# Kernel optimization log

Measured on AMD Instinct MI355X. Metric: run time of the kernel, lower is better.

Reference implementation:

```python
import jax, jax.numpy as jnp
import numpy as np

EMB = 1024
HEADS = 16
HD = EMB // HEADS
EPS = 1e-5

def _ln(x, g, b):
    m = jnp.mean(x, axis=-1, keepdims=True)
    v = jnp.mean((x - m) ** 2, axis=-1, keepdims=True)
    return (x - m) * jax.lax.rsqrt(v + EPS) * g + b

def setup_inputs() -> dict:
    key = jax.random.key(0)
    ks = jax.random.split(key, 12)
    s_in = 1.0 / np.sqrt(EMB)
    s_ff = 1.0 / np.sqrt(4 * EMB)
    return {
        "x": jax.random.normal(ks[0], (2, 2048, EMB), jnp.float32),
        "wq": jax.random.uniform(ks[1], (HEADS, EMB, HD), jnp.float32, -s_in, s_in),
        "wk": jax.random.uniform(ks[2], (HEADS, EMB, HD), jnp.float32, -s_in, s_in),
        "wv": jax.random.uniform(ks[3], (HEADS, EMB, HD), jnp.float32, -s_in, s_in),
        "wo": jax.random.uniform(ks[4], (EMB, EMB), jnp.float32, -s_in, s_in),
        "bo": jax.random.uniform(ks[5], (EMB,), jnp.float32, -s_in, s_in),
        "g1": jnp.ones((EMB,), jnp.float32),
        "b1": jnp.zeros((EMB,), jnp.float32),
        "g2": jnp.ones((EMB,), jnp.float32),
        "b2": jnp.zeros((EMB,), jnp.float32),
        "w1": jax.random.uniform(ks[6], (EMB, 4 * EMB), jnp.float32, -s_in, s_in),
        "bf1": jax.random.uniform(ks[7], (4 * EMB,), jnp.float32, -s_in, s_in),
        "w2": jax.random.uniform(ks[8], (4 * EMB, EMB), jnp.float32, -s_ff, s_ff),
        "bf2": jax.random.uniform(ks[9], (EMB,), jnp.float32, -s_ff, s_ff),
    }

def reference(x, wq, wk, wv, wo, bo, g1, b1, g2, b2, w1, bf1, w2, bf2):
    B, T, C = x.shape
    h = _ln(x, g1, b1)
    # all heads batched: [B,H,T,HD]
    q = jnp.einsum('btc,hcd->bhtd', h, wq)
    k = jnp.einsum('btc,hcd->bhtd', h, wk)
    v = jnp.einsum('btc,hcd->bhtd', h, wv)
    # NOTE: original scales by full emb_size C**-0.5, not head_size
    scores = jnp.einsum('bhtd,bhsd->bhts', q, k) * (C ** -0.5)
    causal = jnp.tril(jnp.ones((T, T), bool))
    scores = jnp.where(causal, scores, -jnp.inf)
    w = jax.nn.softmax(scores, axis=-1)
    attn = jnp.einsum('bhts,bhsd->bhtd', w, v)
    attn = attn.transpose(0, 2, 1, 3).reshape(B, T, C)  # concat heads
    x = x + attn @ wo + bo
    h2 = _ln(x, g2, b2)
    ffn = jax.nn.relu(h2 @ w1 + bf1) @ w2 + bf2
    return x + ffn
```

## Files before the change

### kernel.cpp

```cpp
#include <hip/hip_runtime.h>
#include <hip/hip_bf16.h>

typedef __bf16 bf16x8 __attribute__((ext_vector_type(8)));
typedef float f32x4 __attribute__((ext_vector_type(4)));
typedef short s16x8 __attribute__((ext_vector_type(8)));

#define DEV __device__ __forceinline__

DEV float b2f(unsigned short u) {
  unsigned int x = ((unsigned int)u) << 16;
  return __builtin_bit_cast(float, x);
}
DEV unsigned short f2b(float f) {
  unsigned int x = __builtin_bit_cast(unsigned int, f);
  x += 0x7fffu + ((x >> 16) & 1u);
  return (unsigned short)(x >> 16);
}
DEV unsigned int f2b2(float a, float b) {
  float2 t; t.x = a; t.y = b;
  __hip_bfloat162 v = __float22bfloat162_rn(t);
  unsigned int r;
  __builtin_memcpy(&r, &v, 4);
  return r;
}
DEV f32x4 mfma16(bf16x8 a, bf16x8 b, f32x4 c) {
  return __builtin_amdgcn_mfma_f32_16x16x32_bf16(a, b, c, 0, 0, 0);
}
DEV void gl2lds16(const unsigned short* g, unsigned short* l) {
  __builtin_amdgcn_global_load_lds(
      (const __attribute__((address_space(1))) void*)g,
      (__attribute__((address_space(3))) void*)l, 16, 0, 0);
}

__global__ __launch_bounds__(256)
void transpose_k(const float* __restrict__ in, unsigned short* __restrict__ out,
                 int K, int N, long zin, long zout) {
  __shared__ float tile[32][33];
  in  += (size_t)blockIdx.z * zin;
  out += (size_t)blockIdx.z * zout;
  int n0 = blockIdx.x * 32, k0 = blockIdx.y * 32;
  int tx = threadIdx.x, ty = threadIdx.y;
  #pragma unroll
  for (int i = ty; i < 32; i += 8)
    tile[i][tx] = in[(size_t)(k0 + i) * N + n0 + tx];
  __syncthreads();
  #pragma unroll
  for (int i = ty; i < 32; i += 8)
    out[(size_t)(n0 + i) * K + k0 + tx] = f2b(tile[tx][i]);
}

__global__ __launch_bounds__(256)
void transpose_qkv(const float* __restrict__ wq, const float* __restrict__ wk,
                   const float* __restrict__ wv, unsigned short* __restrict__ out) {
  __shared__ float tile[32][33];
  const int z = blockIdx.z;
  const float* in = (z < 16) ? (wq + (size_t)z * 65536)
                  : (z < 32) ? (wk + (size_t)(z - 16) * 65536)
                             : (wv + (size_t)(z - 32) * 65536);
  unsigned short* o = out + (size_t)z * 65536;
  int n0 = blockIdx.x * 32, k0 = blockIdx.y * 32;
  int tx = threadIdx.x, ty = threadIdx.y;
  #pragma unroll
  for (int i = ty; i < 32; i += 8)
    tile[i][tx] = in[(size_t)(k0 + i) * 64 + n0 + tx];
  __syncthreads();
  #pragma unroll
  for (int i = ty; i < 32; i += 8)
    o[(size_t)(n0 + i) * 1024 + k0 + tx] = f2b(tile[tx][i]);
}

__global__ __launch_bounds__(256)
void ln_kernel(const float* __restrict__ x, const float* __restrict__ g,
               const float* __restrict__ b, unsigned short* __restrict__ o) {
  __shared__ float rs[4];
  __shared__ float rq[4];
  int row = blockIdx.x, tid = threadIdx.x;
  const float* xr = x + (size_t)row * 1024;
  float4 raw = ((const float4*)xr)[tid];
  float s = raw.x + raw.y + raw.z + raw.w;
  float q = raw.x*raw.x + raw.y*raw.y + raw.z*raw.z + raw.w*raw.w;
  #pragma unroll
  for (int off = 32; off > 0; off >>= 1) {
    s += __shfl_down(s, off);
    q += __shfl_down(q, off);
  }
  int wave = tid >> 6;
  if ((tid & 63) == 0) { rs[wave] = s; rq[wave] = q; }
  __syncthreads();
  float ts = rs[0] + rs[1] + rs[2] + rs[3];
  float tq = rq[0] + rq[1] + rq[2] + rq[3];
  float mean = ts * (1.0f/1024.0f);
  float var = tq * (1.0f/1024.0f) - mean*mean;
  float rstd = rsqrtf(var + 1e-5f);
  float4 gr = ((const float4*)g)[tid];
  float4 br = ((const float4*)b)[tid];
  float o0 = (raw.x-mean)*rstd*gr.x + br.x;
  float o1 = (raw.y-mean)*rstd*gr.y + br.y;
  float o2 = (raw.z-mean)*rstd*gr.z + br.z;
  float o3 = (raw.w-mean)*rstd*gr.w + br.w;
  uint2 ov;
  ov.x = f2b2(o0, o1);
  ov.y = f2b2(o2, o3);
  ((uint2*)(o + (size_t)row * 1024))[tid] = ov;
}

template<bool RELU, bool BIAS, bool RESID, bool OUTF32, bool VFUSE>
__global__ __launch_bounds__(256)
void gemm_bt(const unsigned short* __restrict__ A, const unsigned short* __restrict__ Bt,
             const float* __restrict__ bias, const float* __restrict__ resid,
             void* __restrict__ Cv, unsigned short* __restrict__ vT, int M, int N, int K) {
  __shared__ unsigned short As[2][128*32];
  __shared__ unsigned short Bs[2][128*32];
  const int tid = threadIdx.x;
  const int lane = tid & 63;
  const int quad = lane >> 4, l16 = lane & 15;
  const int wave = tid >> 6;
  const int m0 = blockIdx.y * 128, n0 = blockIdx.x * 128;
  const int wm = (wave >> 1) * 64, wn = (wave & 1) * 64;

  f32x4 acc[4][4];
  #pragma unroll
  for (int i = 0; i < 4; ++i)
    #pragma unroll
    for (int j = 0; j < 4; ++j) acc[i][j] = (f32x4){0.f, 0.f, 0.f, 0.f};

  const int srow = tid >> 2;
  const int scol = (tid & 3) * 8;
  const unsigned short* Ab = A + (size_t)m0 * K;
  const unsigned short* Bb = Bt + (size_t)n0 * K;

  auto stage = [&](int buf, int k0) {
    gl2lds16(Ab + (size_t)srow * K + k0 + scol,        &As[buf][tid * 8]);
    gl2lds16(Ab + (size_t)(srow + 64) * K + k0 + scol, &As[buf][2048 + tid * 8]);
    gl2lds16(Bb + (size_t)srow * K + k0 + scol,        &Bs[buf][tid * 8]);
    gl2lds16(Bb + (size_t)(srow + 64) * K + k0 + scol, &Bs[buf][2048 + tid * 8]);
  };

  const int niter = K >> 5;
  stage(0, 0);
  __syncthreads();

  for (int it = 0; it < niter; ++it) {
    const int buf = it & 1;
    if (it + 1 < niter) stage(buf ^ 1, (it + 1) * 32);
    bf16x8 af[4], bfr[4];
    #pragma unroll
    for (int i = 0; i < 4; ++i)
      af[i] = __builtin_bit_cast(bf16x8, *(const s16x8*)&As[buf][(wm + i*16 + l16)*32 + quad*8]);
    #pragma unroll
    for (int j = 0; j < 4; ++j)
      bfr[j] = __builtin_bit_cast(bf16x8, *(const s16x8*)&Bs[buf][(wn + j*16 + l16)*32 + quad*8]);
    #pragma unroll
    for (int i = 0; i < 4; ++i)
      #pragma unroll
      for (int j = 0; j < 4; ++j)
        acc[i][j] = mfma16(af[i], bfr[j], acc[i][j]);
    __syncthreads();
  }

  if (VFUSE && n0 >= 2048) {
    #pragma unroll
    for (int i = 0; i < 4; ++i) {
      const int row = m0 + wm + i*16 + quad*4;
      const int b = row >> 11, tloc = row & 2047;
      #pragma unroll
      for (int j = 0; j < 4; ++j) {
        const int col = n0 + wn + j*16 + l16;
        const int h = (col - 2048) >> 6, d = col & 63;
        ushort4 pk;
        pk.x = f2b(acc[i][j][0]);
        pk.y = f2b(acc[i][j][1]);
        pk.z = f2b(acc[i][j][2]);
        pk.w = f2b(acc[i][j][3]);
        *(ushort4*)&vT[((size_t)((b*16 + h)*64 + d))*2048 + tloc] = pk;
      }
    }
    return;
  }

  #pragma unroll
  for (int i = 0; i < 4; ++i) {
    const int row = m0 + wm + i*16 + quad*4;
    #pragma unroll
    for (int j = 0; j < 4; ++j) {
      const int col = n0 + wn + j*16 + l16;
      float bv = 0.f;
      if (BIAS) bv = bias[col];
      #pragma unroll
      for (int r = 0; r < 4; ++r) {
        float v = acc[i][j][r] + bv;
        if (RESID) v += resid[(size_t)(row + r) * N + col];
        if (RELU) v = fmaxf(v, 0.f);
        if (OUTF32) ((float*)Cv)[(size_t)(row + r) * N + col] = v;
        else ((unsigned short*)Cv)[(size_t)(row + r) * N + col] = f2b(v);
      }
    }
  }
}

__global__ __launch_bounds__(256)
void gemm_n1024(const unsigned short* __restrict__ A, const unsigned short* __restrict__ Bt,
                const float* __restrict__ bias, const float* __restrict__ resid,
                float* __restrict__ C, int M, int N, int K) {
  __shared__ unsigned short As[3][64*64];
  __shared__ unsigned short Bs[3][128*64];
  const int tid = threadIdx.x;
  const int lane = tid & 63;
  const int quad = lane >> 4, l16 = lane & 15;
  const int wave = tid >> 6;
  const int id = blockIdx.x;
  const int xcd = id & 7, i2 = id >> 3;
  const int mt = (xcd << 3) | (i2 >> 3);
  const int nt = i2 & 7;
  const int m0 = mt * 64, n0 = nt * 128;
  const int wm = (wave >> 1) * 32, wn = (wave & 1) * 64;

  f32x4 acc[2][4];
  #pragma unroll
  for (int i = 0; i < 2; ++i)
    #pragma unroll
    for (int j = 0; j < 4; ++j) acc[i][j] = (f32x4){0.f, 0.f, 0.f, 0.f};

  const int srow = tid >> 3;
  const int scc  = ((tid & 7) ^ (srow & 7)) * 8;
  const unsigned short* Ab = A + (size_t)m0 * K;
  const unsigned short* Bb = Bt + (size_t)n0 * K;

  auto stage = [&](int buf, int k0) {
    unsigned short* Ad = &As[buf][0];
    unsigned short* Bd = &Bs[buf][0];
    gl2lds16(Ab + (size_t)srow * K + k0 + scc,         Ad + tid * 8);
    gl2lds16(Ab + (size_t)(srow + 32) * K + k0 + scc,  Ad + 2048 + tid * 8);
    gl2lds16(Bb + (size_t)srow * K + k0 + scc,         Bd + tid * 8);
    gl2lds16(Bb + (size_t)(srow + 32) * K + k0 + scc,  Bd + 2048 + tid * 8);
    gl2lds16(Bb + (size_t)(srow + 64) * K + k0 + scc,  Bd + 4096 + tid * 8);
    gl2lds16(Bb + (size_t)(srow + 96) * K + k0 + scc,  Bd + 6144 + tid * 8);
  };

  const int niter = K >> 6;
  stage(0, 0);
  stage(1, 64);

  int bufc = 0;
  for (int it = 0; it < niter; ++it) {
    if (it + 1 < niter) {
      asm volatile("s_waitcnt vmcnt(6)" ::: "memory");
    } else {
      asm volatile("s_waitcnt vmcnt(0)" ::: "memory");
    }
    __builtin_amdgcn_s_barrier();
    if (it + 2 < niter) {
      int bufn = bufc + 2; if (bufn >= 3) bufn -= 3;
      stage(bufn, (it + 2) * 64);
    }
    const unsigned short* Ar = &As[bufc][0];
    const unsigned short* Br = &Bs[bufc][0];
    #pragma unroll
    for (int s = 0; s < 2; ++s) {
      bf16x8 af[2], bfr[4];
      #pragma unroll
      for (int i = 0; i < 2; ++i) {
        const int R = wm + i*16 + l16;
        af[i] = __builtin_bit_cast(bf16x8,
          *(const s16x8*)&Ar[R*64 + (((s*4 + quad) ^ (R & 7)) * 8)]);
      }
      #pragma unroll
      for (int j = 0; j < 4; ++j) {
        const int R = wn + j*16 + l16;
        bfr[j] = __builtin_bit_cast(bf16x8,
          *(const s16x8*)&Br[R*64 + (((s*4 + quad) ^ (R & 7)) * 8)]);
      }
      #pragma unroll
      for (int i = 0; i < 2; ++i)
        #pragma unroll
        for (int j = 0; j < 4; ++j)
          acc[i][j] = mfma16(af[i], bfr[j], acc[i][j]);
    }
    bufc = (bufc == 2) ? 0 : bufc + 1;
  }

  #pragma unroll
  for (int i = 0; i < 2; ++i) {
    const int row = m0 + wm + i*16 + quad*4;
    #pragma unroll
    for (int j = 0; j < 4; ++j) {
      const int col = n0 + wn + j*16 + l16;
      const float bv = bias[col];
      #pragma unroll
      for (int r = 0; r < 4; ++r)
        C[(size_t)(row + r) * N + col] = acc[i][j][r] + bv + resid[(size_t)(row + r) * N + col];
    }
  }
}

__global__ __launch_bounds__(256)
void attn_kernel(const unsigned short* __restrict__ qkv,
                 const unsigned short* __restrict__ vT,
                 unsigned short* __restrict__ outc) {
  __shared__ unsigned short Ks[2][64*64];
  __shared__ unsigned short Vs[2][64*64];
  __shared__ unsigned short Ps[4*16*72];
  const int tid = threadIdx.x, lane = tid & 63, wave = tid >> 6;
  const int quad = lane >> 4, l16 = lane & 15;
  const int bh = blockIdx.y, b = bh >> 4, h = bh & 15;
  const int jA = blockIdx.x, jB = 31 - jA;
  const size_t tokbase = (size_t)b * 2048 * 3072;
  const unsigned short* Q  = qkv + tokbase + h * 64;
  const unsigned short* Kg = qkv + tokbase + 1024 + h * 64;
  const unsigned short* Vg = vT + (size_t)bh * 64 * 2048;

  const s16x8 ones_s = {0x3F80, 0x3F80, 0x3F80, 0x3F80, 0x3F80, 0x3F80, 0x3F80, 0x3F80};
  const bf16x8 onesf = __builtin_bit_cast(bf16x8, ones_s);

  bf16x8 qf[2][2];
  #pragma unroll
  for (int t = 0; t < 2; ++t) {
    const int qrow = (t ? jB : jA) * 64 + wave * 16 + l16;
    #pragma unroll
    for (int s = 0; s < 2; ++s) {
      s16x8 raw = *(const s16x8*)(Q + (size_t)qrow * 3072 + s * 32 + quad * 8);
      unsigned short* rp = (unsigned short*)&raw;
      #pragma unroll
      for (int j = 0; j < 8; ++j) rp[j] = f2b(b2f(rp[j]) * 0.03125f);
      qf[t][s] = __builtin_bit_cast(bf16x8, raw);
    }
  }

  f32x4 accO[2][4];
  f32x4 accS[2] = {(f32x4){0.f,0.f,0.f,0.f}, (f32x4){0.f,0.f,0.f,0.f}};
  #pragma unroll
  for (int t = 0; t < 2; ++t)
    #pragma unroll
    for (int i = 0; i < 4; ++i) accO[t][i] = (f32x4){0.f, 0.f, 0.f, 0.f};

  const int r8 = lane >> 3;
  const int cs = (((lane & 7) ^ r8) * 8);

  auto stage = [&](int buf, int kv0) {
    #pragma unroll
    for (int i = 0; i < 2; ++i) {
      int row = wave * 16 + i * 8;
      gl2lds16(Kg + (size_t)(kv0 + row + r8) * 3072 + cs, &Ks[buf][row * 64 + lane * 8]);
      gl2lds16(Vg + (size_t)(row + r8) * 2048 + kv0 + cs, &Vs[buf][row * 64 + lane * 8]);
    }
  };

  const int ntile = jB + 1;
  stage(0, 0);
  __syncthreads();

  for (int it = 0; it < ntile; ++it) {
    const int buf = it & 1;
    if (it + 1 < ntile) stage(buf ^ 1, (it + 1) * 64);

    #pragma unroll
    for (int t = 0; t < 2; ++t) {
      const int jT = t ? jB : jA;
      if (it > jT) continue;
      f32x4 sv[4];
      #pragma unroll
      for (int ni = 0; ni < 4; ++ni) {
        sv[ni] = (f32x4){0.f, 0.f, 0.f, 0.f};
        #pragma unroll
        for (int s = 0; s < 2; ++s) {
          bf16x8 kf = __builtin_bit_cast(bf16x8,
            *(const s16x8*)&Ks[buf][(ni*16 + l16)*64 + (((s*4 + quad) ^ (l16 & 7)) * 8)]);
          sv[ni] = mfma16(qf[t][s], kf, sv[ni]);
        }
      }
      if (it == jT) {
        const int rowg = jT*64 + wave*16 + quad*4;
        const int kv0 = it * 64;
        #pragma unroll
        for (int ni = 0; ni < 4; ++ni) {
          const int colg = kv0 + ni*16 + l16;
          #pragma unroll
          for (int r = 0; r < 4; ++r)
            if (colg > rowg + r) sv[ni][r] = -__builtin_inff();
        }
      }
      #pragma unroll
      for (int ni = 0; ni < 4; ++ni) {
        float p0 = __expf(sv[ni][0]);
        float p1 = __expf(sv[ni][1]);
        float p2 = __expf(sv[ni][2]);
        float p3 = __expf(sv[ni][3]);
        unsigned int u01 = f2b2(p0, p1);
        unsigned int u23 = f2b2(p2, p3);
        const int base = wave*1152 + ni*16 + l16;
        Ps[base + (quad*4 + 0)*72] = (unsigned short)u01;
        Ps[base + (quad*4 + 1)*72] = (unsigned short)(u01 >> 16);
        Ps[base + (quad*4 + 2)*72] = (unsigned short)u23;
        Ps[base + (quad*4 + 3)*72] = (unsigned short)(u23 >> 16);
      }
      __asm__ volatile("s_waitcnt lgkmcnt(0)" ::: "memory");
      #pragma unroll
      for (int s = 0; s < 2; ++s) {
        bf16x8 pf = __builtin_bit_cast(bf16x8,
          *(const s16x8*)&Ps[wave*1152 + l16*72 + s*32 + quad*8]);
        accS[t] = mfma16(pf, onesf, accS[t]);
        #pragma unroll
        for (int ni = 0; ni < 4; ++ni) {
          bf16x8 vf = __builtin_bit_cast(bf16x8,
            *(const s16x8*)&Vs[buf][(ni*16 + l16)*64 + (((s*4 + quad) ^ (l16 & 7)) * 8)]);
          accO[t][ni] = mfma16(pf, vf, accO[t][ni]);
        }
      }
    }
    __syncthreads();
  }

  #pragma unroll
  for (int t = 0; t < 2; ++t) {
    const int rowg = (t ? jB : jA)*64 + wave*16 + quad*4;
    float inv[4];
    #pragma unroll
    for (int r = 0; r < 4; ++r) inv[r] = __builtin_amdgcn_rcpf(accS[t][r]);
    #pragma unroll
    for (int ni = 0; ni < 4; ++ni)
      #pragma unroll
      for (int r = 0; r < 4; ++r)
        outc[(size_t)(b*2048 + rowg + r) * 1024 + h*64 + ni*16 + l16]
          = f2b(accO[t][ni][r] * inv[r]);
  }
}

extern "C" void kernel_launch(void* const* d_in, const int* in_sizes, int n_in,
                              void* d_out, int out_size, void* d_ws, size_t ws_size,
                              hipStream_t stream) {
  (void)in_sizes; (void)n_in; (void)out_size; (void)ws_size;
  const float* x   = (const float*)d_in[0];
  const float* wq  = (const float*)d_in[1];
  const float* wk  = (const float*)d_in[2];
  const float* wv  = (const float*)d_in[3];
  const float* wo  = (const float*)d_in[4];
  const float* bo  = (const float*)d_in[5];
  const float* g1  = (const float*)d_in[6];
  const float* b1  = (const float*)d_in[7];
  const float* g2  = (const float*)d_in[8];
  const float* b2  = (const float*)d_in[9];
  const float* w1  = (const float*)d_in[10];
  const float* bf1 = (const float*)d_in[11];
  const float* w2  = (const float*)d_in[12];
  const float* bf2 = (const float*)d_in[13];
  float* out = (float*)d_out;

  unsigned short* ws    = (unsigned short*)d_ws;
  unsigned short* wqkvt = ws;
  unsigned short* wot   = wqkvt + 3*1024*1024;
  unsigned short* w1t   = wot   + 1024*1024;
  unsigned short* w2t   = w1t   + 4096*1024;
  unsigned short* hbuf  = w2t   + 4096*1024;
  unsigned short* qkvb  = hbuf  + 4096*1024;
  unsigned short* attnb = qkvb  + (size_t)4096*3072;
  float*          x2b   = (float*)(attnb + 4096*1024);
  unsigned short* vTb   = (unsigned short*)x2b;
  unsigned short* midb  = qkvb;

  dim3 tb(32, 8);
  transpose_qkv<<<dim3(2,32,48), tb, 0, stream>>>(wq, wk, wv, wqkvt);
  transpose_k<<<dim3(32,32,1),  tb, 0, stream>>>(wo, wot, 1024, 1024, 0, 0);
  transpose_k<<<dim3(128,32,1), tb, 0, stream>>>(w1, w1t, 1024, 4096, 0, 0);
  transpose_k<<<dim3(32,128,1), tb, 0, stream>>>(w2, w2t, 4096, 1024, 0, 0);

  ln_kernel<<<4096, 256, 0, stream>>>(x, g1, b1, hbuf);
  gemm_bt<false,false,false,false,true><<<dim3(24,32), 256, 0, stream>>>(
      hbuf, wqkvt, nullptr, nullptr, qkvb, vTb, 4096, 3072, 1024);
  attn_kernel<<<dim3(16,32), 256, 0, stream>>>(qkvb, vTb, attnb);
  gemm_n1024<<<512, 256, 0, stream>>>(attnb, wot, bo, x, x2b, 4096, 1024, 1024);
  ln_kernel<<<4096, 256, 0, stream>>>(x2b, g2, b2, hbuf);
  gemm_bt<true,true,false,false,false><<<dim3(32,32), 256, 0, stream>>>(
      hbuf, w1t, bf1, nullptr, midb, nullptr, 4096, 4096, 1024);
  gemm_n1024<<<512, 256, 0, stream>>>(midb, w2t, bf2, x2b, out, 4096, 1024, 4096);
}
```

Baseline: 345.0 us.

## Replace QKV and FFN1 GEMMs with 256x256-tile 8-wave pipelined kernel

Swaps the 128x128 double-buffered GEMM for a 256x256-tile kernel with 8 waves, a 4-stage LDS ring fed by split partial stages, explicit vmcnt waits and barriers, and s_setprio around the MFMA blocks. LDS reads use an XOR swizzle to avoid bank conflicts, and the block order is remapped so work is spread across XCDs. The goal is higher MFMA utilisation through more reuse per tile and overlap of global loads with compute. In exchange, the 192- and 256-block grids may leave CUs underfilled, and the hand-written waitcnt logic is fragile.

```diff
diff --git a/kernel.cpp b/kernel.cpp
--- a/kernel.cpp
+++ b/kernel.cpp
@@ -104,95 +104,132 @@
   ((uint2*)(o + (size_t)row * 1024))[tid] = ov;
 }
 
-template<bool RELU, bool BIAS, bool RESID, bool OUTF32, bool VFUSE>
-__global__ __launch_bounds__(256)
-void gemm_bt(const unsigned short* __restrict__ A, const unsigned short* __restrict__ Bt,
-             const float* __restrict__ bias, const float* __restrict__ resid,
-             void* __restrict__ Cv, unsigned short* __restrict__ vT, int M, int N, int K) {
-  __shared__ unsigned short As[2][128*32];
-  __shared__ unsigned short Bs[2][128*32];
+template<bool RELU, bool BIAS, bool VFUSE>
+__global__ __launch_bounds__(512, 2)
+void gemm8p(const unsigned short* __restrict__ A, const unsigned short* __restrict__ Bt,
+            const float* __restrict__ bias, void* __restrict__ Cv,
+            unsigned short* __restrict__ vT, int NTn, int N, int K) {
+  __shared__ unsigned short As[4][256*32];
+  __shared__ unsigned short Bs[4][256*32];
   const int tid = threadIdx.x;
-  const int lane = tid & 63;
+  const int lane = tid & 63, wave = tid >> 6;
   const int quad = lane >> 4, l16 = lane & 15;
-  const int wave = tid >> 6;
-  const int m0 = blockIdx.y * 128, n0 = blockIdx.x * 128;
-  const int wm = (wave >> 1) * 64, wn = (wave & 1) * 64;
-
-  f32x4 acc[4][4];
-  #pragma unroll
-  for (int i = 0; i < 4; ++i)
+  const int wm = wave >> 2, wn = wave & 3;
+  const int nwg = gridDim.x;
+  const int id = blockIdx.x;
+  const int id2 = (id & 7) * (nwg >> 3) + (id >> 3);
+  const int mt = id2 / NTn, nt = id2 % NTn;
+  const int m0 = mt * 256, n0 = nt * 256;
+
+  f32x4 acc[8][4];
+  #pragma unroll
+  for (int i = 0; i < 8; ++i)
     #pragma unroll
     for (int j = 0; j < 4; ++j) acc[i][j] = (f32x4){0.f, 0.f, 0.f, 0.f};
 
   const int srow = tid >> 2;
-  const int scol = (tid & 3) * 8;
+  const int scc  = (((tid & 3) ^ ((srow >> 1) & 3)) * 8);
   const unsigned short* Ab = A + (size_t)m0 * K;
   const unsigned short* Bb = Bt + (size_t)n0 * K;
 
-  auto stage = [&](int buf, int k0) {
-    gl2lds16(Ab + (size_t)srow * K + k0 + scol,        &As[buf][tid * 8]);
-    gl2lds16(Ab + (size_t)(srow + 64) * K + k0 + scol, &As[buf][2048 + tid * 8]);
-    gl2lds16(Bb + (size_t)srow * K + k0 + scol,        &Bs[buf][tid * 8]);
-    gl2lds16(Bb + (size_t)(srow + 64) * K + k0 + scol, &Bs[buf][2048 + tid * 8]);
+  const int NT = K >> 5;
+  const int H  = NT << 2;
+
+  auto stage = [&](int h) {
+    const int Tt = h >> 2, part = h & 3, kk = Tt << 5;
+    const int buf = Tt & 3;
+    if (part == 0)
+      gl2lds16(Ab + (size_t)srow * K + kk + scc,         &As[buf][tid * 8]);
+    else if (part == 1)
+      gl2lds16(Ab + (size_t)(srow + 128) * K + kk + scc, &As[buf][4096 + tid * 8]);
+    else if (part == 2)
+      gl2lds16(Bb + (size_t)srow * K + kk + scc,         &Bs[buf][tid * 8]);
+    else
+      gl2lds16(Bb + (size_t)(srow + 128) * K + kk + scc, &Bs[buf][4096 + tid * 8]);
   };
 
-  const int niter = K >> 5;
-  stage(0, 0);
-  __syncthreads();
-
-  for (int it = 0; it < niter; ++it) {
-    const int buf = it & 1;
-    if (it + 1 < niter) stage(buf ^ 1, (it + 1) * 32);
-    bf16x8 af[4], bfr[4];
-    #pragma unroll
-    for (int i = 0; i < 4; ++i)
-      af[i] = __builtin_bit_cast(bf16x8, *(const s16x8*)&As[buf][(wm + i*16 + l16)*32 + quad*8]);
-    #pragma unroll
-    for (int j = 0; j < 4; ++j)
-      bfr[j] = __builtin_bit_cast(bf16x8, *(const s16x8*)&Bs[buf][(wn + j*16 + l16)*32 + quad*8]);
-    #pragma unroll
-    for (int i = 0; i < 4; ++i)
+  #pragma unroll
+  for (int h = 0; h < 10; ++h) stage(h);
+  asm volatile("s_waitcnt vmcnt(6)" ::: "memory");
+  asm volatile("s_barrier" ::: "memory");
+
+  const int qsw = (quad ^ ((l16 >> 1) & 3)) * 8;
+  const int arow0 = wm * 128 + l16;
+  const int brow0 = wn * 64 + l16;
+
+  for (int T = 0; T < NT; ++T) {
+    const int buf = T & 3;
+    bf16x8 bq[4];
+    {
+      bf16x8 af[4];
+      #pragma unroll
+      for (int i = 0; i < 4; ++i)
+        af[i] = __builtin_bit_cast(bf16x8,
+          *(const s16x8*)&As[buf][(arow0 + i*16)*32 + qsw]);
       #pragma unroll
       for (int j = 0; j < 4; ++j)
-        acc[i][j] = mfma16(af[i], bfr[j], acc[i][j]);
-    __syncthreads();
-  }
-
-  if (VFUSE && n0 >= 2048) {
-    #pragma unroll
-    for (int i = 0; i < 4; ++i) {
-      const int row = m0 + wm + i*16 + quad*4;
-      const int b = row >> 11, tloc = row & 2047;
-      #pragma unroll
-      for (int j = 0; j < 4; ++j) {
-        const int col = n0 + wn + j*16 + l16;
+        bq[j] = __builtin_bit_cast(bf16x8,
+          *(const s16x8*)&Bs[buf][(brow0 + j*16)*32 + qsw]);
+      const int h = 4*T + 10;
+      if (h < H)     stage(h);
+      if (h + 1 < H) stage(h + 1);
+      asm volatile("s_barrier" ::: "memory");
+      __builtin_amdgcn_s_setprio(1);
+      #pragma unroll
+      for (int i = 0; i < 4; ++i)
+        #pragma unroll
+        for (int j = 0; j < 4; ++j)
+          acc[i][j] = mfma16(af[i], bq[j], acc[i][j]);
+      __builtin_amdgcn_s_setprio(0);
+      asm volatile("s_barrier" ::: "memory");
+    }
+    {
+      bf16x8 af[4];
+      #pragma unroll
+      for (int i = 0; i < 4; ++i)
+        af[i] = __builtin_bit_cast(bf16x8,
+          *(const s16x8*)&As[buf][(arow0 + 64 + i*16)*32 + qsw]);
+      const int h = 4*T + 12;
+      if (h < H)     stage(h);
+      if (h + 1 < H) stage(h + 1);
+      if (T + 3 < NT)      { asm volatile("s_waitcnt vmcnt(6)" ::: "memory"); }
+      else if (T + 2 < NT) { asm volatile("s_waitcnt vmcnt(4)" ::: "memory"); }
+      else if (T + 1 < NT) { asm volatile("s_waitcnt vmcnt(0)" ::: "memory"); }
+      asm volatile("s_barrier" ::: "memory");
+      __builtin_amdgcn_s_setprio(1);
+      #pragma unroll
+      for (int i = 0; i < 4; ++i)
+        #pragma unroll
+        for (int j = 0; j < 4; ++j)
+          acc[4 + i][j] = mfma16(af[i], bq[j], acc[4 + i][j]);
+      __builtin_amdgcn_s_setprio(0);
+      asm volatile("s_barrier" ::: "memory");
+    }
+  }
+
+  #pragma unroll
+  for (int ii = 0; ii < 8; ++ii) {
+    const int row = m0 + wm*128 + ii*16 + quad*4;
+    #pragma unroll
+    for (int j = 0; j < 4; ++j) {
+      const int col = n0 + wn*64 + j*16 + l16;
+      if (VFUSE && col >= 2048) {
+        const int b = row >> 11, tloc = row & 2047;
         const int h = (col - 2048) >> 6, d = col & 63;
         ushort4 pk;
-        pk.x = f2b(acc[i][j][0]);
-        pk.y = f2b(acc[i][j][1]);
-        pk.z = f2b(acc[i][j][2]);
-        pk.w = f2b(acc[i][j][3]);
+        pk.x = f2b(acc[ii][j][0]);
+        pk.y = f2b(acc[ii][j][1]);
+        pk.z = f2b(acc[ii][j][2]);
+        pk.w = f2b(acc[ii][j][3]);
         *(ushort4*)&vT[((size_t)((b*16 + h)*64 + d))*2048 + tloc] = pk;
-      }
-    }
-    return;
-  }
-
-  #pragma unroll
-  for (int i = 0; i < 4; ++i) {
-    const int row = m0 + wm + i*16 + quad*4;
-    #pragma unroll
-    for (int j = 0; j < 4; ++j) {
-      const int col = n0 + wn + j*16 + l16;
-      float bv = 0.f;
-      if (BIAS) bv = bias[col];
-      #pragma unroll
-      for (int r = 0; r < 4; ++r) {
-        float v = acc[i][j][r] + bv;
-        if (RESID) v += resid[(size_t)(row + r) * N + col];
-        if (RELU) v = fmaxf(v, 0.f);
-        if (OUTF32) ((float*)Cv)[(size_t)(row + r) * N + col] = v;
-        else ((unsigned short*)Cv)[(size_t)(row + r) * N + col] = f2b(v);
+      } else {
+        float bv = BIAS ? bias[col] : 0.f;
+        #pragma unroll
+        for (int r = 0; r < 4; ++r) {
+          float v = acc[ii][j][r] + bv;
+          if (RELU) v = fmaxf(v, 0.f);
+          ((unsigned short*)Cv)[(size_t)(row + r) * N + col] = f2b(v);
+        }
       }
     }
   }
@@ -464,12 +501,12 @@
   transpose_k<<<dim3(32,128,1), tb, 0, stream>>>(w2, w2t, 4096, 1024, 0, 0);
 
   ln_kernel<<<4096, 256, 0, stream>>>(x, g1, b1, hbuf);
-  gemm_bt<false,false,false,false,true><<<dim3(24,32), 256, 0, stream>>>(
-      hbuf, wqkvt, nullptr, nullptr, qkvb, vTb, 4096, 3072, 1024);
+  gemm8p<false,false,true><<<192, 512, 0, stream>>>(
+      hbuf, wqkvt, nullptr, qkvb, vTb, 12, 3072, 1024);
   attn_kernel<<<dim3(16,32), 256, 0, stream>>>(qkvb, vTb, attnb);
   gemm_n1024<<<512, 256, 0, stream>>>(attnb, wot, bo, x, x2b, 4096, 1024, 1024);
   ln_kernel<<<4096, 256, 0, stream>>>(x2b, g2, b2, hbuf);
-  gemm_bt<true,true,false,false,false><<<dim3(32,32), 256, 0, stream>>>(
-      hbuf, w1t, bf1, nullptr, midb, nullptr, 4096, 4096, 1024);
+  gemm8p<true,true,false><<<256, 512, 0, stream>>>(
+      hbuf, w1t, bf1, midb, nullptr, 16, 4096, 1024);
   gemm_n1024<<<512, 256, 0, stream>>>(midb, w2t, bf2, x2b, out, 4096, 1024, 4096);
 }
```

Result: no change. 343.5 us (-0.5%).
